# Optimization experiments

Hardware: AMD Instinct MI355X
Metric: run time of the kernel (lower is better)

Reference implementation:

```python
import jax, jax.numpy as jnp
import numpy as np

N, D_IN, UNITS = 8192, 4096, 4096

def ste_sign(k):
    # larq ste_sign forward: sign with sign(0) -> +1
    return jnp.where(k >= 0, 1.0, -1.0).astype(k.dtype)

def setup_inputs() -> dict:
    key = jax.random.key(0)
    kx, kk = jax.random.split(key)
    x = jax.random.normal(kx, (N, D_IN), dtype=jnp.float32)
    kernel = jax.random.normal(kk, (D_IN, UNITS), dtype=jnp.float32)
    return {"x": x, "kernel": kernel}

def reference(x, kernel):
    # y = x @ sign(kernel); the `+ reduce_sum(x)*0` in the original is a no-op
    return x @ ste_sign(kernel)
```

## Files before the change

kernel.cpp:

```cpp
#include <hip/hip_runtime.h>
#include <stdint.h>

typedef __attribute__((ext_vector_type(8))) __bf16 bf16x8;
typedef __attribute__((ext_vector_type(4))) float f32x4;

__device__ inline unsigned short f32_to_bf16_rne(float f) {
  union { float f; uint32_t u; } c; c.f = f;
  uint32_t u = c.u;
  uint32_t r = (u + 0x7FFFu + ((u >> 16) & 1u)) >> 16;
  return (unsigned short)r;
}

__global__ __launch_bounds__(256) void convert_x_kernel(const float* __restrict__ X,
                                                        unsigned short* __restrict__ A,
                                                        size_t n) {
  size_t i = (size_t)blockIdx.x * 256 + threadIdx.x;
  size_t stride = (size_t)gridDim.x * 256;
  for (size_t e = i * 4; e < n; e += stride * 4) {
    const float4 v = *reinterpret_cast<const float4*>(X + e);
    ushort4 o;
    o.x = f32_to_bf16_rne(v.x);
    o.y = f32_to_bf16_rne(v.y);
    o.z = f32_to_bf16_rne(v.z);
    o.w = f32_to_bf16_rne(v.w);
    *reinterpret_cast<ushort4*>(A + e) = o;
  }
}

__global__ __launch_bounds__(256) void sign_transpose_kernel(const float* __restrict__ Km,
                                                             unsigned short* __restrict__ Bt,
                                                             int K, int N) {
  __shared__ unsigned short tile[64][65];
  const int k0 = blockIdx.x * 64;
  const int n0 = blockIdx.y * 64;
  const int t = threadIdx.x;
#pragma unroll
  for (int i = 0; i < 16; ++i) {
    int idx = t + i * 256;
    int kk = idx >> 6, nn = idx & 63;
    float v = Km[(size_t)(k0 + kk) * N + (n0 + nn)];
    tile[kk][nn] = (v >= 0.0f) ? (unsigned short)0x3F80u : (unsigned short)0xBF80u;
  }
  __syncthreads();
#pragma unroll
  for (int i = 0; i < 16; ++i) {
    int idx = t + i * 256;
    int nn = idx >> 6, kk = idx & 63;
    Bt[(size_t)(n0 + nn) * K + (k0 + kk)] = tile[kk][nn];
  }
}


__device__ __forceinline__ void stage_mat(const unsigned short* __restrict__ G,
                                          size_t grow0, int K, int k0,
                                          unsigned short* lds_wave_base,
                                          int tid) {
#pragma unroll
  for (int i = 0; i < 2; ++i) {
    const int row = i * 128 + (tid >> 2);
    const int srcslot = (tid & 3) ^ ((row >> 1) & 3);
    const unsigned short* ga = G + (grow0 + row) * (size_t)K + k0 + srcslot * 8;
    __builtin_amdgcn_global_load_lds(
        (const __attribute__((address_space(1))) void*)ga,
        (__attribute__((address_space(3))) void*)(lds_wave_base + i * 4096),
        16, 0, 0);
  }
}

#define GEMM_ITER(T, AFC, BFC, AFN, BFN)                                              \
  {                                                                                   \
    const int cb = ((T) & 3) * 16384;                                                 \
    const int ts = ((T) + 3 < NTt) ? ((T) + 3) : (NTt - 1);                           \
    const int tb = (ts & 3) * 16384;                                                  \
    bf16x8 af1[4];                                                                    \
    _Pragma("unroll")                                                                 \
    for (int mi = 0; mi < 4; ++mi)                                                    \
      af1[mi] = *reinterpret_cast<const bf16x8*>(&lds[cb + aoff + 2048 + mi * 512]);  \
    stage_mat(A, a_row0, K, ts * 32, &lds[tb + wv * 512], tid);                       \
    __builtin_amdgcn_sched_barrier(0);                                                \
    __builtin_amdgcn_s_setprio(1);                                                    \
    _Pragma("unroll")                                                                 \
    for (int mi = 0; mi < 4; ++mi)                                                    \
      _Pragma("unroll")                                                               \
      for (int ni = 0; ni < 4; ++ni)                                                  \
        acc[mi][ni] =                                                                 \
            __builtin_amdgcn_mfma_f32_16x16x32_bf16(AFC[mi], BFC[ni], acc[mi][ni], 0, 0, 0); \
    __builtin_amdgcn_s_setprio(0);                                                    \
    __builtin_amdgcn_sched_barrier(0);                                                \
    const int nb = ((T) + 1 < NTt) ? ((((T) + 1) & 3) * 16384) : cb;                  \
    _Pragma("unroll")                                                                 \
    for (int ni = 0; ni < 4; ++ni)                                                    \
      BFN[ni] = *reinterpret_cast<const bf16x8*>(&lds[nb + boff + ni * 512]);         \
    _Pragma("unroll")                                                                 \
    for (int mi = 0; mi < 4; ++mi)                                                    \
      AFN[mi] = *reinterpret_cast<const bf16x8*>(&lds[nb + aoff + mi * 512]);         \
    stage_mat(Bt, b_row0, K, ts * 32, &lds[tb + 8192 + wv * 512], tid);               \
    __builtin_amdgcn_sched_barrier(0);                                                \
    __builtin_amdgcn_s_setprio(1);                                                    \
    _Pragma("unroll")                                                                 \
    for (int mi = 0; mi < 4; ++mi)                                                    \
      _Pragma("unroll")                                                               \
      for (int ni = 0; ni < 4; ++ni)                                                  \
        acc[4 + mi][ni] =                                                             \
            __builtin_amdgcn_mfma_f32_16x16x32_bf16(af1[mi], BFC[ni], acc[4 + mi][ni], 0, 0, 0); \
    __builtin_amdgcn_s_setprio(0);                                                    \
    asm volatile("s_waitcnt vmcnt(4)\n" ::: "memory");                                \
    __builtin_amdgcn_s_barrier();                                                     \
  }

__global__ __launch_bounds__(512, 2) void gemm_bf16_256(const unsigned short* __restrict__ A,
                                                        const unsigned short* __restrict__ Bt,
                                                        float* __restrict__ C,
                                                        int M, int N, int K) {
  __shared__ unsigned short lds[4 * 16384];

  const int nBN = N >> 8;
  const int nwg = gridDim.x;
  const int bid = blockIdx.x;
  int swz = bid;
  if ((nwg & 7) == 0) {
    const int q = nwg >> 3;
    swz = (bid & 7) * q + (bid >> 3);
  }
  const size_t a_row0 = (size_t)(swz / nBN) * 256;
  const size_t b_row0 = (size_t)(swz % nBN) * 256;

  const int tid = threadIdx.x;
  const int wv = tid >> 6, ln = tid & 63;
  const int llo = ln & 15, lhi = ln >> 4;
  const int wr = wv >> 2, wc = wv & 3;
  const int sA = lhi ^ ((llo >> 1) & 3);

  const int aoff = (wr * 128 + llo) * 32 + sA * 8;
  const int boff = 8192 + (wc * 64 + llo) * 32 + sA * 8;

  const int NTt = K >> 5;

  f32x4 acc[8][4];
#pragma unroll
  for (int i = 0; i < 8; ++i)
#pragma unroll
    for (int j = 0; j < 4; ++j) acc[i][j] = (f32x4){0.f, 0.f, 0.f, 0.f};

#pragma unroll
  for (int tt = 0; tt < 3; ++tt) {
    stage_mat(A, a_row0, K, tt * 32, &lds[tt * 16384 + wv * 512], tid);
    stage_mat(Bt, b_row0, K, tt * 32, &lds[tt * 16384 + 8192 + wv * 512], tid);
  }
  asm volatile("s_waitcnt vmcnt(4)\n" ::: "memory");
  __builtin_amdgcn_s_barrier();

  bf16x8 af0_a[4], bfr_a[4], af0_b[4], bfr_b[4];
#pragma unroll
  for (int ni = 0; ni < 4; ++ni)
    bfr_a[ni] = *reinterpret_cast<const bf16x8*>(&lds[boff + ni * 512]);
#pragma unroll
  for (int mi = 0; mi < 4; ++mi)
    af0_a[mi] = *reinterpret_cast<const bf16x8*>(&lds[aoff + mi * 512]);

  for (int t = 0; t < NTt; t += 2) {
    GEMM_ITER(t, af0_a, bfr_a, af0_b, bfr_b)
    GEMM_ITER(t + 1, af0_b, bfr_b, af0_a, bfr_a)
  }

#pragma unroll
  for (int mi = 0; mi < 8; ++mi) {
#pragma unroll
    for (int ni = 0; ni < 4; ++ni) {
      const size_t col = b_row0 + wc * 64 + ni * 16 + llo;
      const size_t rbase = a_row0 + wr * 128 + mi * 16 + lhi * 4;
#pragma unroll
      for (int j = 0; j < 4; ++j)
        C[(rbase + j) * (size_t)N + col] = acc[mi][ni][j];
    }
  }
}

__global__ __launch_bounds__(256) void gemm_f32_fallback(const float* __restrict__ X,
                                                         const float* __restrict__ Km,
                                                         float* __restrict__ C,
                                                         int M, int N, int K) {
  __shared__ float As[64][16];
  __shared__ float Bs[16][65];
  const int nBN = N / 64;
  const int bm = blockIdx.x / nBN;
  const int bn = blockIdx.x % nBN;
  const int t = threadIdx.x;
  const int tx = t & 15, ty = t >> 4;
  float acc[4][4] = {};
  for (int kb = 0; kb < K; kb += 16) {
#pragma unroll
    for (int i = 0; i < 4; ++i) {
      int e = t + i * 256;
      int r = e >> 4, c = e & 15;
      As[r][c] = X[(size_t)(bm * 64 + r) * K + kb + c];
      int rk = e >> 6, cn = e & 63;
      float v = Km[(size_t)(kb + rk) * N + bn * 64 + cn];
      Bs[rk][cn] = (v >= 0.f) ? 1.f : -1.f;
    }
    __syncthreads();
#pragma unroll
    for (int kk = 0; kk < 16; ++kk) {
      float a[4], b[4];
#pragma unroll
      for (int r = 0; r < 4; ++r) a[r] = As[ty * 4 + r][kk];
#pragma unroll
      for (int c = 0; c < 4; ++c) b[c] = Bs[kk][tx * 4 + c];
#pragma unroll
      for (int r = 0; r < 4; ++r)
#pragma unroll
        for (int c = 0; c < 4; ++c) acc[r][c] += a[r] * b[c];
    }
    __syncthreads();
  }
#pragma unroll
  for (int r = 0; r < 4; ++r)
#pragma unroll
    for (int c = 0; c < 4; ++c)
      C[(size_t)(bm * 64 + ty * 4 + r) * N + bn * 64 + tx * 4 + c] = acc[r][c];
}

extern "C" void kernel_launch(void* const* d_in, const int* in_sizes, int n_in,
                              void* d_out, int out_size, void* d_ws, size_t ws_size,
                              hipStream_t stream) {
  const float* x = (const float*)d_in[0];
  const float* kern = (const float*)d_in[1];
  float* out = (float*)d_out;

  const int K = 4096;
  const int N = 4096;
  const int M = in_sizes[0] / K;

  const size_t a_bytes = (size_t)M * K * 2;
  const size_t b_bytes = (size_t)N * K * 2;

  if (ws_size >= a_bytes + b_bytes && (M % 256) == 0 && (N % 256) == 0 && (K % 128) == 0) {
    unsigned short* A = (unsigned short*)d_ws;
    unsigned short* Bt = (unsigned short*)((char*)d_ws + a_bytes);
    convert_x_kernel<<<2048, 256, 0, stream>>>(x, A, (size_t)M * K);
    sign_transpose_kernel<<<dim3(K / 64, N / 64), 256, 0, stream>>>(kern, Bt, K, N);
    gemm_bf16_256<<<(M / 256) * (N / 256), 512, 0, stream>>>(A, Bt, out, M, N, K);
  } else {
    gemm_f32_fallback<<<(M / 64) * (N / 64), 256, 0, stream>>>(x, kern, out, M, N, K);
  }
}
```

Measured before the change: 266.4 us.

## Switch GEMM inner loop from 16x16x32 to 32x32x16 bf16 MFMA tiles

Replaces the 16x16x32 MFMA with 32x32x16 MFMA instructions. The per-wave fragment layout, LDS read addressing (XOR swizzled slot within a row), accumulator shapes and the output store mapping all change to match. The larger MFMA tile reads fewer fragment registers per flop and issues fewer MFMA instructions, aiming for higher matrix-core throughput. The risks are a different LDS bank-conflict pattern and a changed register footprint under the 2-wave occupancy bound.

```diff
diff --git a/kernel.cpp b/kernel.cpp
--- a/kernel.cpp
+++ b/kernel.cpp
@@ -2,7 +2,7 @@
 #include <stdint.h>
 
 typedef __attribute__((ext_vector_type(8))) __bf16 bf16x8;
-typedef __attribute__((ext_vector_type(4))) float f32x4;
+typedef __attribute__((ext_vector_type(16))) float f32x16;
 
 __device__ inline unsigned short f32_to_bf16_rne(float f) {
   union { float f; uint32_t u; } c; c.f = f;
@@ -72,37 +72,47 @@
     const int cb = ((T) & 3) * 16384;                                                 \
     const int ts = ((T) + 3 < NTt) ? ((T) + 3) : (NTt - 1);                           \
     const int tb = (ts & 3) * 16384;                                                  \
+    const int nb = ((T) + 1 < NTt) ? ((((T) + 1) & 3) * 16384) : cb;                  \
     bf16x8 af1[4];                                                                    \
     _Pragma("unroll")                                                                 \
-    for (int mi = 0; mi < 4; ++mi)                                                    \
-      af1[mi] = *reinterpret_cast<const bf16x8*>(&lds[cb + aoff + 2048 + mi * 512]);  \
+    for (int j = 0; j < 4; ++j)                                                       \
+      af1[j] = *reinterpret_cast<const bf16x8*>(                                      \
+          &lds[(cb + aoff + (2 + (j >> 1)) * 1024) ^ ((j & 1) << 4)]);                \
+    _Pragma("unroll")                                                                 \
+    for (int j = 0; j < 2; ++j)                                                       \
+      BFN[j] = *reinterpret_cast<const bf16x8*>(&lds[(nb + boff) ^ ((j & 1) << 4)]);  \
     stage_mat(A, a_row0, K, ts * 32, &lds[tb + wv * 512], tid);                       \
     __builtin_amdgcn_sched_barrier(0);                                                \
     __builtin_amdgcn_s_setprio(1);                                                    \
     _Pragma("unroll")                                                                 \
-    for (int mi = 0; mi < 4; ++mi)                                                    \
+    for (int ks = 0; ks < 2; ++ks)                                                    \
       _Pragma("unroll")                                                               \
-      for (int ni = 0; ni < 4; ++ni)                                                  \
-        acc[mi][ni] =                                                                 \
-            __builtin_amdgcn_mfma_f32_16x16x32_bf16(AFC[mi], BFC[ni], acc[mi][ni], 0, 0, 0); \
+      for (int rb = 0; rb < 2; ++rb)                                                  \
+        _Pragma("unroll")                                                             \
+        for (int cbn = 0; cbn < 2; ++cbn)                                             \
+          acc[rb][cbn] = __builtin_amdgcn_mfma_f32_32x32x16_bf16(                     \
+              AFC[2 * rb + ks], BFC[2 * cbn + ks], acc[rb][cbn], 0, 0, 0);            \
     __builtin_amdgcn_s_setprio(0);                                                    \
     __builtin_amdgcn_sched_barrier(0);                                                \
-    const int nb = ((T) + 1 < NTt) ? ((((T) + 1) & 3) * 16384) : cb;                  \
-    _Pragma("unroll")                                                                 \
-    for (int ni = 0; ni < 4; ++ni)                                                    \
-      BFN[ni] = *reinterpret_cast<const bf16x8*>(&lds[nb + boff + ni * 512]);         \
-    _Pragma("unroll")                                                                 \
-    for (int mi = 0; mi < 4; ++mi)                                                    \
-      AFN[mi] = *reinterpret_cast<const bf16x8*>(&lds[nb + aoff + mi * 512]);         \
+    _Pragma("unroll")                                                                 \
+    for (int j = 2; j < 4; ++j)                                                       \
+      BFN[j] = *reinterpret_cast<const bf16x8*>(                                      \
+          &lds[(nb + boff + 1024) ^ ((j & 1) << 4)]);                                 \
+    _Pragma("unroll")                                                                 \
+    for (int j = 0; j < 4; ++j)                                                       \
+      AFN[j] = *reinterpret_cast<const bf16x8*>(                                      \
+          &lds[(nb + aoff + (j >> 1) * 1024) ^ ((j & 1) << 4)]);                      \
     stage_mat(Bt, b_row0, K, ts * 32, &lds[tb + 8192 + wv * 512], tid);               \
     __builtin_amdgcn_sched_barrier(0);                                                \
     __builtin_amdgcn_s_setprio(1);                                                    \
     _Pragma("unroll")                                                                 \
-    for (int mi = 0; mi < 4; ++mi)                                                    \
+    for (int ks = 0; ks < 2; ++ks)                                                    \
       _Pragma("unroll")                                                               \
-      for (int ni = 0; ni < 4; ++ni)                                                  \
-        acc[4 + mi][ni] =                                                             \
-            __builtin_amdgcn_mfma_f32_16x16x32_bf16(af1[mi], BFC[ni], acc[4 + mi][ni], 0, 0, 0); \
+      for (int rb = 0; rb < 2; ++rb)                                                  \
+        _Pragma("unroll")                                                             \
+        for (int cbn = 0; cbn < 2; ++cbn)                                             \
+          acc[2 + rb][cbn] = __builtin_amdgcn_mfma_f32_32x32x16_bf16(                 \
+              af1[2 * rb + ks], BFC[2 * cbn + ks], acc[2 + rb][cbn], 0, 0, 0);        \
     __builtin_amdgcn_s_setprio(0);                                                    \
     asm volatile("s_waitcnt vmcnt(4)\n" ::: "memory");                                \
     __builtin_amdgcn_s_barrier();                                                     \
@@ -127,20 +137,22 @@
 
   const int tid = threadIdx.x;
   const int wv = tid >> 6, ln = tid & 63;
-  const int llo = ln & 15, lhi = ln >> 4;
+  const int r5 = ln & 31, hi = ln >> 5;
   const int wr = wv >> 2, wc = wv & 3;
-  const int sA = lhi ^ ((llo >> 1) & 3);
-
-  const int aoff = (wr * 128 + llo) * 32 + sA * 8;
-  const int boff = 8192 + (wc * 64 + llo) * 32 + sA * 8;
+
+  const int slot0 = (hi ^ ((r5 >> 1) & 3)) * 8;
+  const int aoff = (wr * 128 + r5) * 32 + slot0;
+  const int boff = 8192 + (wc * 64 + r5) * 32 + slot0;
 
   const int NTt = K >> 5;
 
-  f32x4 acc[8][4];
-#pragma unroll
-  for (int i = 0; i < 8; ++i)
-#pragma unroll
-    for (int j = 0; j < 4; ++j) acc[i][j] = (f32x4){0.f, 0.f, 0.f, 0.f};
+  f32x16 acc[4][2];
+#pragma unroll
+  for (int i = 0; i < 4; ++i)
+#pragma unroll
+    for (int j = 0; j < 2; ++j)
+#pragma unroll
+      for (int r = 0; r < 16; ++r) acc[i][j][r] = 0.f;
 
 #pragma unroll
   for (int tt = 0; tt < 3; ++tt) {
@@ -152,11 +164,11 @@
 
   bf16x8 af0_a[4], bfr_a[4], af0_b[4], bfr_b[4];
 #pragma unroll
-  for (int ni = 0; ni < 4; ++ni)
-    bfr_a[ni] = *reinterpret_cast<const bf16x8*>(&lds[boff + ni * 512]);
-#pragma unroll
-  for (int mi = 0; mi < 4; ++mi)
-    af0_a[mi] = *reinterpret_cast<const bf16x8*>(&lds[aoff + mi * 512]);
+  for (int j = 0; j < 4; ++j)
+    bfr_a[j] = *reinterpret_cast<const bf16x8*>(&lds[(boff + (j >> 1) * 1024) ^ ((j & 1) << 4)]);
+#pragma unroll
+  for (int j = 0; j < 4; ++j)
+    af0_a[j] = *reinterpret_cast<const bf16x8*>(&lds[(aoff + (j >> 1) * 1024) ^ ((j & 1) << 4)]);
 
   for (int t = 0; t < NTt; t += 2) {
     GEMM_ITER(t, af0_a, bfr_a, af0_b, bfr_b)
@@ -164,14 +176,16 @@
   }
 
 #pragma unroll
-  for (int mi = 0; mi < 8; ++mi) {
-#pragma unroll
-    for (int ni = 0; ni < 4; ++ni) {
-      const size_t col = b_row0 + wc * 64 + ni * 16 + llo;
-      const size_t rbase = a_row0 + wr * 128 + mi * 16 + lhi * 4;
-#pragma unroll
-      for (int j = 0; j < 4; ++j)
-        C[(rbase + j) * (size_t)N + col] = acc[mi][ni][j];
+  for (int rb = 0; rb < 4; ++rb) {
+#pragma unroll
+    for (int cbn = 0; cbn < 2; ++cbn) {
+      const size_t col = b_row0 + wc * 64 + cbn * 32 + r5;
+      const size_t rbase = a_row0 + wr * 128 + rb * 32 + 4 * hi;
+#pragma unroll
+      for (int r = 0; r < 16; ++r) {
+        const size_t row = rbase + (r & 3) + 8 * (r >> 2);
+        C[row * (size_t)N + col] = acc[rb][cbn][r];
+      }
     }
   }
 }
```

Measured after the change: 294.6 us. +10.6%, slower.
